# Optimization experiments

Measured on AMD Instinct MI355X. Metric: run time of the kernel, lower is better.

Reference implementation:

```python
import jax, jax.numpy as jnp
import numpy as np

B, C, IC, H, W = 4, 64, 32, 128, 128


def _conv1x1(x, w, b):
    # x: [b,c,h,w], w: [o,c], b: [o]
    return jnp.einsum('bchw,oc->bohw', x, w) + b[None, :, None, None]


def _maxpool2(x):
    b, c, h, w = x.shape
    return x.reshape(b, c, h // 2, 2, w // 2, 2).max(axis=(3, 5))


def setup_inputs() -> dict:
    key = jax.random.key(0)
    ks = jax.random.split(key, 11)
    sc = 0.05
    return {
        'target': jax.random.normal(ks[0], (B, C, H, W), jnp.float32),
        'ref': jax.random.normal(ks[1], (B, C, H, W), jnp.float32),
        'ref_align': jax.random.normal(ks[2], (B, C, H, W), jnp.float32),
        'theta_w': jax.random.normal(ks[3], (IC, C), jnp.float32) * sc,
        'theta_b': jax.random.normal(ks[4], (IC,), jnp.float32) * sc,
        'phi_w': jax.random.normal(ks[5], (IC, C), jnp.float32) * sc,
        'phi_b': jax.random.normal(ks[6], (IC,), jnp.float32) * sc,
        'g_w': jax.random.normal(ks[7], (IC, C), jnp.float32) * sc,
        'g_b': jax.random.normal(ks[8], (IC,), jnp.float32) * sc,
        'W_w': jax.random.normal(ks[9], (C, IC), jnp.float32) * sc,
        'W_b': jax.random.normal(ks[10], (C,), jnp.float32) * sc,
    }


def reference(target, ref, ref_align, theta_w, theta_b, phi_w, phi_b, g_w, g_b, W_w, W_b):
    b, c, h, w = target.shape
    N = h * w
    # phi, g: 1x1 conv then 2x2 maxpool -> [b, ic, N/4]
    phi = _maxpool2(_conv1x1(ref, phi_w, phi_b)).reshape(b, -1, N // 4)
    g = _maxpool2(_conv1x1(ref_align, g_w, g_b)).reshape(b, -1, N // 4)
    theta = _conv1x1(target, theta_w, theta_b).reshape(b, -1, N)  # [b, ic, N]
    # softmax-free attention: s [b, N, N/4]
    s = jnp.einsum('bin,bim->bnm', theta, phi) / N
    y = jnp.einsum('bnm,bim->bin', s, g)  # [b, ic, N]
    y = y.reshape(b, -1, h, w)
    return _conv1x1(y, W_w, W_b) + target
```

## Files before the change

kernel.cpp:

```cpp
#include <hip/hip_runtime.h>

#define Bn  4
#define Cc  64
#define ICc 32
#define Hh  128
#define Ww  128
#define Nn  (Hh*Ww)
#define Hp  (Hh/2)
#define Wp  (Ww/2)
#define PAD 66

__global__ __launch_bounds__(256) void zero_A(float* __restrict__ A)
{
    ((float4*)A)[blockIdx.x * 256 + threadIdx.x] = make_float4(0.f, 0.f, 0.f, 0.f);
}

__global__ __launch_bounds__(1024) void conv_gram_kernel(
    const float* __restrict__ ref, const float* __restrict__ ref_align,
    const float* __restrict__ phi_w, const float* __restrict__ phi_b,
    const float* __restrict__ g_w,   const float* __restrict__ g_b,
    float* __restrict__ A)
{
    __shared__ float swT[2][Cc * ICc];
    __shared__ float sb[2][ICc];
    __shared__ float tile[2][ICc][PAD];

    const int b = blockIdx.y, ph = blockIdx.x, tid = threadIdx.x;

    for (int idx = tid; idx < Cc * ICc; idx += 1024) {
        const int c = idx >> 5, i = idx & 31;
        swT[0][idx] = phi_w[i * Cc + c];
        swT[1][idx] = g_w[i * Cc + c];
    }
    if (tid < ICc) { sb[0][tid] = phi_b[tid]; sb[1][tid] = g_b[tid]; }
    __syncthreads();

    {
        const int r   = tid & 1;
        const int img = (tid >> 1) & 1;
        const int pw  = (tid >> 2) & 63;
        const int icg = (tid >> 8) * 8;
        const float* in = img ? ref_align : ref;
        const float2* xrow = (const float2*)in
                           + ((size_t)(b * Cc * Hh) + 2 * ph + r) * (Ww / 2);
        const int cs2 = (Hh * Ww) / 2;
        const float* wimg = swT[img];

        float acc0[8], acc1[8];
        #pragma unroll
        for (int i = 0; i < 8; ++i) { acc0[i] = sb[img][icg + i]; acc1[i] = acc0[i]; }

        #pragma unroll 8
        for (int c = 0; c < Cc; ++c) {
            const float2 v = xrow[c * cs2 + pw];
            const float4* w4 = (const float4*)(wimg + c * ICc + icg);
            #pragma unroll
            for (int q = 0; q < 2; ++q) {
                const float4 w = w4[q];
                acc0[4*q+0] = fmaf(w.x, v.x, acc0[4*q+0]);
                acc1[4*q+0] = fmaf(w.x, v.y, acc1[4*q+0]);
                acc0[4*q+1] = fmaf(w.y, v.x, acc0[4*q+1]);
                acc1[4*q+1] = fmaf(w.y, v.y, acc1[4*q+1]);
                acc0[4*q+2] = fmaf(w.z, v.x, acc0[4*q+2]);
                acc1[4*q+2] = fmaf(w.z, v.y, acc1[4*q+2]);
                acc0[4*q+3] = fmaf(w.w, v.x, acc0[4*q+3]);
                acc1[4*q+3] = fmaf(w.w, v.y, acc1[4*q+3]);
            }
        }

        #pragma unroll
        for (int i = 0; i < 8; ++i) {
            float mx = fmaxf(acc0[i], acc1[i]);
            mx = fmaxf(mx, __shfl_xor(mx, 1, 64));
            if (r == 0) tile[img][icg + i][pw] = mx;
        }
    }
    __syncthreads();

    {
        const int i = tid >> 5;
        const int j = tid & 31;
        float s = 0.f;
        #pragma unroll 8
        for (int p = 0; p < Wp / 2; ++p) {
            const float2 gv = *(const float2*)&tile[1][i][2 * p];
            const float2 pv = *(const float2*)&tile[0][j][2 * p];
            s = fmaf(gv.x, pv.x, fmaf(gv.y, pv.y, s));
        }
        atomicAdd(A + ((size_t)b * ICc + i) * ICc + j, s);
    }
}

__global__ __launch_bounds__(256) void apply_kernel(
    const float* __restrict__ x, const float* __restrict__ A,
    const float* __restrict__ theta_w, const float* __restrict__ theta_b,
    const float* __restrict__ W_w,     const float* __restrict__ W_b,
    float* __restrict__ out)
{
    const int b  = blockIdx.y;
    const int ob = blockIdx.z * 8;

    __shared__ float sA[ICc * ICc];
    __shared__ float sT[8 * ICc];
    __shared__ float sM[8 * Cc];
    __shared__ float sv[8];

    for (int idx = threadIdx.x; idx < ICc * ICc; idx += 256)
        sA[idx] = A[(size_t)b * ICc * ICc + idx];
    __syncthreads();

    {
        const int ol = threadIdx.x >> 5, j = threadIdx.x & 31;
        const float* wr = W_w + (ob + ol) * ICc;
        float t = 0.f;
        #pragma unroll
        for (int i = 0; i < ICc; ++i) t = fmaf(wr[i], sA[i * ICc + j], t);
        sT[ol * ICc + j] = t;
    }
    __syncthreads();

    const float invN = 1.f / (float)Nn;
    for (int idx = threadIdx.x; idx < 8 * Cc; idx += 256) {
        const int ol = idx >> 6, c = idx & 63;
        float s = 0.f;
        #pragma unroll
        for (int j = 0; j < ICc; ++j) s = fmaf(sT[ol * ICc + j], theta_w[j * Cc + c], s);
        sM[idx] = s * invN + ((ob + ol) == c ? 1.f : 0.f);
    }
    if (threadIdx.x < 8) {
        float v = 0.f;
        #pragma unroll
        for (int j = 0; j < ICc; ++j) v = fmaf(sT[threadIdx.x * ICc + j], theta_b[j], v);
        sv[threadIdx.x] = v * invN + W_b[ob + threadIdx.x];
    }
    __syncthreads();

    const int n2 = blockIdx.x * 256 + threadIdx.x;
    const float2* xb  = (const float2*)(x + (size_t)b * Cc * Nn);
    float2*       ob2 = (float2*)(out + (size_t)b * Cc * Nn);

    float ax[8], ay[8];
    #pragma unroll
    for (int i = 0; i < 8; ++i) { ax[i] = sv[i]; ay[i] = sv[i]; }

    #pragma unroll 8
    for (int c = 0; c < Cc; ++c) {
        float2 xv = xb[c * (Nn / 2) + n2];
        #pragma unroll
        for (int i = 0; i < 8; ++i) {
            float w = sM[i * Cc + c];
            ax[i] = fmaf(w, xv.x, ax[i]);
            ay[i] = fmaf(w, xv.y, ay[i]);
        }
    }

    #pragma unroll
    for (int i = 0; i < 8; ++i) {
        float2 o2; o2.x = ax[i]; o2.y = ay[i];
        ob2[(ob + i) * (Nn / 2) + n2] = o2;
    }
}

extern "C" void kernel_launch(void* const* d_in, const int* in_sizes, int n_in,
                              void* d_out, int out_size, void* d_ws, size_t ws_size,
                              hipStream_t stream) {
    const float* target    = (const float*)d_in[0];
    const float* ref       = (const float*)d_in[1];
    const float* ref_align = (const float*)d_in[2];
    const float* theta_w   = (const float*)d_in[3];
    const float* theta_b   = (const float*)d_in[4];
    const float* phi_w     = (const float*)d_in[5];
    const float* phi_b     = (const float*)d_in[6];
    const float* g_w       = (const float*)d_in[7];
    const float* g_b       = (const float*)d_in[8];
    const float* W_w       = (const float*)d_in[9];
    const float* W_b       = (const float*)d_in[10];
    float* out = (float*)d_out;

    float* A = (float*)d_ws;

    zero_A<<<4, 256, 0, stream>>>(A);
    conv_gram_kernel<<<dim3(Hp, Bn), 1024, 0, stream>>>(ref, ref_align,
                                                        phi_w, phi_b, g_w, g_b, A);
    apply_kernel<<<dim3(Nn / 512, Bn, 8), 256, 0, stream>>>(target, A,
                                                            theta_w, theta_b,
                                                            W_w, W_b, out);
}
```

Measured before the change: 147.0 us.

## Precompute transposed weights, rework conv-gram threading, vectorize apply with XCD-aware mapping

Measured after the change: 135.4 us. 7.9% less time.

```diff
diff --git a/kernel.cpp b/kernel.cpp
--- a/kernel.cpp
+++ b/kernel.cpp
@@ -10,84 +10,83 @@
 #define Wp  (Ww/2)
 #define PAD 66
 
-__global__ __launch_bounds__(256) void zero_A(float* __restrict__ A)
+
+__global__ __launch_bounds__(256) void init_ws(
+    const float* __restrict__ phi_w, const float* __restrict__ g_w,
+    float* __restrict__ ws)
 {
-    ((float4*)A)[blockIdx.x * 256 + threadIdx.x] = make_float4(0.f, 0.f, 0.f, 0.f);
-}
-
-__global__ __launch_bounds__(1024) void conv_gram_kernel(
+    const int gid = blockIdx.x * 256 + threadIdx.x;
+    if (gid < 4096) {
+        ws[gid] = 0.f;
+    } else {
+        const int idx = gid - 4096;
+        const int img = idx >> 11;
+        const int rem = idx & 2047;
+        const int c = rem >> 5, i = rem & 31;
+        ws[gid] = (img ? g_w : phi_w)[i * Cc + c];
+    }
+}
+
+__global__ __launch_bounds__(512) void conv_gram_kernel(
     const float* __restrict__ ref, const float* __restrict__ ref_align,
-    const float* __restrict__ phi_w, const float* __restrict__ phi_b,
-    const float* __restrict__ g_w,   const float* __restrict__ g_b,
+    const float* __restrict__ phi_b, const float* __restrict__ g_b,
+    const float* __restrict__ wT,
     float* __restrict__ A)
 {
-    __shared__ float swT[2][Cc * ICc];
-    __shared__ float sb[2][ICc];
     __shared__ float tile[2][ICc][PAD];
 
     const int b = blockIdx.y, ph = blockIdx.x, tid = threadIdx.x;
-
-    for (int idx = tid; idx < Cc * ICc; idx += 1024) {
-        const int c = idx >> 5, i = idx & 31;
-        swT[0][idx] = phi_w[i * Cc + c];
-        swT[1][idx] = g_w[i * Cc + c];
-    }
-    if (tid < ICc) { sb[0][tid] = phi_b[tid]; sb[1][tid] = g_b[tid]; }
+    const int pw  = tid & 63;
+    const int icg = __builtin_amdgcn_readfirstlane(((tid >> 6) & 3) * 8);
+    const int img = __builtin_amdgcn_readfirstlane(tid >> 8);
+
+    const float* in = img ? ref_align : ref;
+    const float2* xrow0 = (const float2*)in + ((size_t)(b * Cc * Hh) + 2 * ph)     * (Ww / 2);
+    const float2* xrow1 = (const float2*)in + ((size_t)(b * Cc * Hh) + 2 * ph + 1) * (Ww / 2);
+    const int cs2 = (Hh * Ww) / 2;
+    const float* wt   = wT + img * (Cc * ICc) + icg;
+    const float* bias = (img ? g_b : phi_b) + icg;
+
+    float a00[8], a01[8], a10[8], a11[8];
+    #pragma unroll
+    for (int i = 0; i < 8; ++i) { a00[i] = a01[i] = a10[i] = a11[i] = 0.f; }
+
+    #pragma unroll 8
+    for (int c = 0; c < Cc; ++c) {
+        const float2 v0 = xrow0[c * cs2 + pw];
+        const float2 v1 = xrow1[c * cs2 + pw];
+        const float* wr = wt + c * ICc;
+        #pragma unroll
+        for (int i = 0; i < 8; ++i) {
+            const float w = wr[i];
+            a00[i] = fmaf(w, v0.x, a00[i]);
+            a01[i] = fmaf(w, v0.y, a01[i]);
+            a10[i] = fmaf(w, v1.x, a10[i]);
+            a11[i] = fmaf(w, v1.y, a11[i]);
+        }
+    }
+
+    #pragma unroll
+    for (int i = 0; i < 8; ++i) {
+        const float mx = fmaxf(fmaxf(a00[i], a01[i]), fmaxf(a10[i], a11[i]));
+        tile[img][icg + i][pw] = mx + bias[i];
+    }
     __syncthreads();
 
     {
-        const int r   = tid & 1;
-        const int img = (tid >> 1) & 1;
-        const int pw  = (tid >> 2) & 63;
-        const int icg = (tid >> 8) * 8;
-        const float* in = img ? ref_align : ref;
-        const float2* xrow = (const float2*)in
-                           + ((size_t)(b * Cc * Hh) + 2 * ph + r) * (Ww / 2);
-        const int cs2 = (Hh * Ww) / 2;
-        const float* wimg = swT[img];
-
-        float acc0[8], acc1[8];
-        #pragma unroll
-        for (int i = 0; i < 8; ++i) { acc0[i] = sb[img][icg + i]; acc1[i] = acc0[i]; }
-
-        #pragma unroll 8
-        for (int c = 0; c < Cc; ++c) {
-            const float2 v = xrow[c * cs2 + pw];
-            const float4* w4 = (const float4*)(wimg + c * ICc + icg);
-            #pragma unroll
-            for (int q = 0; q < 2; ++q) {
-                const float4 w = w4[q];
-                acc0[4*q+0] = fmaf(w.x, v.x, acc0[4*q+0]);
-                acc1[4*q+0] = fmaf(w.x, v.y, acc1[4*q+0]);
-                acc0[4*q+1] = fmaf(w.y, v.x, acc0[4*q+1]);
-                acc1[4*q+1] = fmaf(w.y, v.y, acc1[4*q+1]);
-                acc0[4*q+2] = fmaf(w.z, v.x, acc0[4*q+2]);
-                acc1[4*q+2] = fmaf(w.z, v.y, acc1[4*q+2]);
-                acc0[4*q+3] = fmaf(w.w, v.x, acc0[4*q+3]);
-                acc1[4*q+3] = fmaf(w.w, v.y, acc1[4*q+3]);
-            }
-        }
-
-        #pragma unroll
-        for (int i = 0; i < 8; ++i) {
-            float mx = fmaxf(acc0[i], acc1[i]);
-            mx = fmaxf(mx, __shfl_xor(mx, 1, 64));
-            if (r == 0) tile[img][icg + i][pw] = mx;
-        }
-    }
-    __syncthreads();
-
-    {
-        const int i = tid >> 5;
-        const int j = tid & 31;
-        float s = 0.f;
+        const int j  = tid & 31;
+        const int i0 = tid >> 5;
+        float s0 = 0.f, s1 = 0.f;
         #pragma unroll 8
         for (int p = 0; p < Wp / 2; ++p) {
-            const float2 gv = *(const float2*)&tile[1][i][2 * p];
             const float2 pv = *(const float2*)&tile[0][j][2 * p];
-            s = fmaf(gv.x, pv.x, fmaf(gv.y, pv.y, s));
+            const float2 g0 = *(const float2*)&tile[1][i0][2 * p];
+            const float2 g1 = *(const float2*)&tile[1][i0 + 16][2 * p];
+            s0 = fmaf(g0.x, pv.x, fmaf(g0.y, pv.y, s0));
+            s1 = fmaf(g1.x, pv.x, fmaf(g1.y, pv.y, s1));
         }
-        atomicAdd(A + ((size_t)b * ICc + i) * ICc + j, s);
+        atomicAdd(A + ((size_t)b * ICc + i0)      * ICc + j, s0);
+        atomicAdd(A + ((size_t)b * ICc + i0 + 16) * ICc + j, s1);
     }
 }
 
@@ -97,12 +96,19 @@
     const float* __restrict__ W_w,     const float* __restrict__ W_b,
     float* __restrict__ out)
 {
-    const int b  = blockIdx.y;
-    const int ob = blockIdx.z * 8;
-
-    __shared__ float sA[ICc * ICc];
-    __shared__ float sT[8 * ICc];
-    __shared__ float sM[8 * Cc];
+    const int id  = blockIdx.x;
+    const int xcd = id & 7;
+    const int t   = id >> 3;
+    const int s   = t & 7;
+    const int ghi = t >> 3;
+    const int g   = ghi * 8 + xcd;
+    const int nx  = g & 15;
+    const int b   = g >> 4;
+    const int ob  = s * 8;
+
+    __shared__ __align__(16) float sA[ICc * ICc];
+    __shared__ __align__(16) float sT[8 * ICc];
+    __shared__ __align__(16) float sM[8 * Cc];
     __shared__ float sv[8];
 
     for (int idx = threadIdx.x; idx < ICc * ICc; idx += 256)
@@ -112,20 +118,20 @@
     {
         const int ol = threadIdx.x >> 5, j = threadIdx.x & 31;
         const float* wr = W_w + (ob + ol) * ICc;
-        float t = 0.f;
-        #pragma unroll
-        for (int i = 0; i < ICc; ++i) t = fmaf(wr[i], sA[i * ICc + j], t);
-        sT[ol * ICc + j] = t;
+        float tacc = 0.f;
+        #pragma unroll
+        for (int i = 0; i < ICc; ++i) tacc = fmaf(wr[i], sA[i * ICc + j], tacc);
+        sT[ol * ICc + j] = tacc;
     }
     __syncthreads();
 
     const float invN = 1.f / (float)Nn;
     for (int idx = threadIdx.x; idx < 8 * Cc; idx += 256) {
         const int ol = idx >> 6, c = idx & 63;
-        float s = 0.f;
-        #pragma unroll
-        for (int j = 0; j < ICc; ++j) s = fmaf(sT[ol * ICc + j], theta_w[j * Cc + c], s);
-        sM[idx] = s * invN + ((ob + ol) == c ? 1.f : 0.f);
+        float sacc = 0.f;
+        #pragma unroll
+        for (int j = 0; j < ICc; ++j) sacc = fmaf(sT[ol * ICc + j], theta_w[j * Cc + c], sacc);
+        sM[idx] = sacc * invN + ((ob + ol) == c ? 1.f : 0.f);
     }
     if (threadIdx.x < 8) {
         float v = 0.f;
@@ -135,30 +141,39 @@
     }
     __syncthreads();
 
-    const int n2 = blockIdx.x * 256 + threadIdx.x;
-    const float2* xb  = (const float2*)(x + (size_t)b * Cc * Nn);
-    float2*       ob2 = (float2*)(out + (size_t)b * Cc * Nn);
-
-    float ax[8], ay[8];
-    #pragma unroll
-    for (int i = 0; i < 8; ++i) { ax[i] = sv[i]; ay[i] = sv[i]; }
-
-    #pragma unroll 8
-    for (int c = 0; c < Cc; ++c) {
-        float2 xv = xb[c * (Nn / 2) + n2];
+    const int n4 = nx * 256 + threadIdx.x;
+    const float4* xb  = (const float4*)(x   + (size_t)b * Cc * Nn);
+    float4*       ov4 = (float4*)      (out + (size_t)b * Cc * Nn);
+
+    float4 acc[8];
+    #pragma unroll
+    for (int i = 0; i < 8; ++i) acc[i] = make_float4(sv[i], sv[i], sv[i], sv[i]);
+
+#define FMA4(a, wv, xv) { (a).x = fmaf((wv), (xv).x, (a).x); \
+                          (a).y = fmaf((wv), (xv).y, (a).y); \
+                          (a).z = fmaf((wv), (xv).z, (a).z); \
+                          (a).w = fmaf((wv), (xv).w, (a).w); }
+
+    #pragma unroll 2
+    for (int c4 = 0; c4 < Cc / 4; ++c4) {
+        float4 xv0 = xb[(c4 * 4 + 0) * (Nn / 4) + n4];
+        float4 xv1 = xb[(c4 * 4 + 1) * (Nn / 4) + n4];
+        float4 xv2 = xb[(c4 * 4 + 2) * (Nn / 4) + n4];
+        float4 xv3 = xb[(c4 * 4 + 3) * (Nn / 4) + n4];
         #pragma unroll
         for (int i = 0; i < 8; ++i) {
-            float w = sM[i * Cc + c];
-            ax[i] = fmaf(w, xv.x, ax[i]);
-            ay[i] = fmaf(w, xv.y, ay[i]);
+            const float4 w = *(const float4*)&sM[i * Cc + c4 * 4];
+            FMA4(acc[i], w.x, xv0);
+            FMA4(acc[i], w.y, xv1);
+            FMA4(acc[i], w.z, xv2);
+            FMA4(acc[i], w.w, xv3);
         }
     }
-
-    #pragma unroll
-    for (int i = 0; i < 8; ++i) {
-        float2 o2; o2.x = ax[i]; o2.y = ay[i];
-        ob2[(ob + i) * (Nn / 2) + n2] = o2;
-    }
+#undef FMA4
+
+    #pragma unroll
+    for (int i = 0; i < 8; ++i)
+        ov4[(size_t)(ob + i) * (Nn / 4) + n4] = acc[i];
 }
 
 extern "C" void kernel_launch(void* const* d_in, const int* in_sizes, int n_in,
@@ -177,12 +192,13 @@
     const float* W_b       = (const float*)d_in[10];
     float* out = (float*)d_out;
 
-    float* A = (float*)d_ws;
-
-    zero_A<<<4, 256, 0, stream>>>(A);
-    conv_gram_kernel<<<dim3(Hp, Bn), 1024, 0, stream>>>(ref, ref_align,
-                                                        phi_w, phi_b, g_w, g_b, A);
-    apply_kernel<<<dim3(Nn / 512, Bn, 8), 256, 0, stream>>>(target, A,
-                                                            theta_w, theta_b,
-                                                            W_w, W_b, out);
-}
+    float* ws = (float*)d_ws;
+    float* A  = ws;
+    float* wT = ws + 4096;
+
+    init_ws<<<32, 256, 0, stream>>>(phi_w, g_w, ws);
+    conv_gram_kernel<<<dim3(Hp, Bn), 512, 0, stream>>>(ref, ref_align,
+                                                       phi_b, g_b, wT, A);
+    apply_kernel<<<512, 256, 0, stream>>>(target, A, theta_w, theta_b,
+                                          W_w, W_b, out);
+}
```
